# Kernel optimization log

Hardware: AMD Instinct MI355X
Metric: run time of the kernel (lower is better)

The kernel has to match this reference:

```python
import jax, jax.numpy as jnp
import numpy as np

# --- constants (match init_kwargs / input_specs) ---
N_NODES = 32768   # total nodes
N_EDGES = 262144  # total edges (avg degree 8)
B = 512           # number of graphs
D = 64            # node feature / hidden dim (scalar irreps width)
DE = 16           # edge attribute dim
NEXP = 8          # num_experts
K = 2             # top-k


def setup_inputs() -> dict:
    key = jax.random.key(0)
    ks = jax.random.split(key, 20)
    x = jax.random.normal(ks[0], (N_NODES, D), dtype=jnp.float32)
    edge_src = jax.random.randint(ks[1], (N_EDGES,), 0, N_NODES, dtype=jnp.int32)
    edge_dst = jax.random.randint(ks[2], (N_EDGES,), 0, N_NODES, dtype=jnp.int32)
    edge_attr = jax.random.normal(ks[3], (N_EDGES, DE), dtype=jnp.float32)
    # sorted graph ids, every graph non-empty (64 nodes each)
    batch = jnp.repeat(jnp.arange(B, dtype=jnp.int32), N_NODES // B)
    s = 1.0 / np.sqrt(D)
    se = 1.0 / np.sqrt(DE)
    # embedding GNN params
    emb_We = jax.random.normal(ks[4], (DE, D), dtype=jnp.float32) * se
    emb_W1 = jax.random.normal(ks[5], (D, D), dtype=jnp.float32) * s
    emb_W2 = jax.random.normal(ks[6], (D, D), dtype=jnp.float32) * s
    emb_b = jnp.zeros((D,), dtype=jnp.float32)
    # gating network
    Wg = jax.random.normal(ks[7], (D, NEXP), dtype=jnp.float32) * s
    bg = jnp.zeros((NEXP,), dtype=jnp.float32)
    # stacked expert params [NEXP, ...]
    ex_We = jax.random.normal(ks[8], (NEXP, DE, D), dtype=jnp.float32) * se
    ex_W1 = jax.random.normal(ks[9], (NEXP, D, D), dtype=jnp.float32) * s
    ex_W2 = jax.random.normal(ks[10], (NEXP, D, D), dtype=jnp.float32) * s
    ex_b = jnp.zeros((NEXP, D), dtype=jnp.float32)
    ex_Wout = jax.random.normal(ks[11], (NEXP, D, 1), dtype=jnp.float32) * s
    ex_bout = jnp.zeros((NEXP, 1), dtype=jnp.float32)
    return {
        "x": x, "edge_attr": edge_attr,
        "emb_We": emb_We, "emb_W1": emb_W1, "emb_W2": emb_W2, "emb_b": emb_b,
        "Wg": Wg, "bg": bg,
        "ex_We": ex_We, "ex_W1": ex_W1, "ex_W2": ex_W2, "ex_b": ex_b,
        "ex_Wout": ex_Wout, "ex_bout": ex_bout,
        "edge_src": edge_src, "edge_dst": edge_dst, "batch": batch,
    }


def _gnn_embed(x, edge_attr, We, W1, W2, b, src, dst, batch):
    # edge-gated messages: gather x[src], modulate by projected edge attrs, scatter to dst
    msg = x[src] * (edge_attr @ We)                          # [E, D]
    agg = jax.ops.segment_sum(msg, dst, num_segments=N_NODES)  # [N, D]
    h = jax.nn.relu(x @ W1 + agg @ W2 + b)                   # [N, D]
    # mean pooling per graph
    gsum = jax.ops.segment_sum(h, batch, num_segments=B)      # [B, D]
    cnt = jax.ops.segment_sum(jnp.ones((N_NODES, 1), h.dtype), batch, num_segments=B)
    return gsum / jnp.maximum(cnt, 1.0)                      # [B, D]


def _expert(x, edge_attr, We, W1, W2, b, Wout, bout, src, dst, batch):
    emb = _gnn_embed(x, edge_attr, We, W1, W2, b, src, dst, batch)
    return emb @ Wout + bout                                  # [B, 1]


def reference(x, edge_attr, emb_We, emb_W1, emb_W2, emb_b, Wg, bg,
              ex_We, ex_W1, ex_W2, ex_b, ex_Wout, ex_bout,
              edge_src, edge_dst, batch):
    # 1) graph embeddings via embedding GNN
    graph_emb = _gnn_embed(x, edge_attr, emb_We, emb_W1, emb_W2, emb_b,
                           edge_src, edge_dst, batch)          # [B, D]
    # 2) gating: softmax over experts, top-k, renormalize
    routing_weights = jax.nn.softmax(graph_emb @ Wg + bg, axis=1)  # [B, NEXP]
    top_k_weights, top_k_indices = jax.lax.top_k(routing_weights, K)
    norm_top_k = jax.nn.softmax(top_k_weights, axis=1)             # [B, K]
    # 3) dispatch: run every expert on the full batch (vectorized equivalent of
    #    the per-expert masked sub-batch loop), then gather routed outputs
    expert_outs = jax.vmap(
        lambda We, W1, W2, b, Wo, bo: _expert(
            x, edge_attr, We, W1, W2, b, Wo, bo, edge_src, edge_dst, batch)
    )(ex_We, ex_W1, ex_W2, ex_b, ex_Wout, ex_bout)             # [NEXP, B, 1]
    per_graph = expert_outs[:, :, 0].T                         # [B, NEXP]
    gathered = jnp.take_along_axis(per_graph, top_k_indices, axis=1)  # [B, K]
    # 4) weighted combine
    final_output = jnp.sum(gathered * norm_top_k, axis=1, keepdims=True)  # [B, 1]
    return final_output, routing_weights
```

## Files before the change

### kernel.cpp

```cpp
#include <hip/hip_runtime.h>

#define N_NODES 32768
#define N_EDGES 262144
#define NB      512
#define D       64
#define DE      16
#define NEXP    8

typedef __attribute__((ext_vector_type(8))) short  short8v;
typedef __attribute__((ext_vector_type(4))) float  floatx4;

static __device__ __forceinline__ unsigned short f2bf(float f) {
  unsigned int u = __float_as_uint(f);
  u += 0x7FFFu + ((u >> 16) & 1u);
  return (unsigned short)(u >> 16);
}


__global__ void hist_kernel(const int* __restrict__ dst, int* __restrict__ counts) {
  int i = blockIdx.x * blockDim.x + threadIdx.x;
  if (i < N_EDGES) atomicAdd(&counts[dst[i]], 1);
}

__global__ void scan1_kernel(const int* __restrict__ counts, int* __restrict__ offsets,
                             int* __restrict__ bsums) {
  __shared__ int sm[256];
  int t = threadIdx.x, i = blockIdx.x * 256 + t;
  int v = counts[i];
  sm[t] = v;
  __syncthreads();
  for (int off = 1; off < 256; off <<= 1) {
    int u = (t >= off) ? sm[t - off] : 0;
    __syncthreads();
    sm[t] += u;
    __syncthreads();
  }
  offsets[i] = sm[t] - v;
  if (t == 255) bsums[blockIdx.x] = sm[255];
}

__global__ void scan2_kernel(int* __restrict__ bsums) {
  __shared__ int sm[128];
  int t = threadIdx.x;
  int v = bsums[t];
  sm[t] = v;
  __syncthreads();
  for (int off = 1; off < 128; off <<= 1) {
    int u = (t >= off) ? sm[t - off] : 0;
    __syncthreads();
    sm[t] += u;
    __syncthreads();
  }
  bsums[t] = sm[t] - v;
}

__global__ void scan3_kernel(int* __restrict__ offsets, const int* __restrict__ bsums,
                             int* __restrict__ cursor) {
  int i = blockIdx.x * 256 + threadIdx.x;
  int v = offsets[i] + bsums[blockIdx.x];
  offsets[i] = v;
  cursor[i]  = v;
  if (i == 0) offsets[N_NODES] = N_EDGES;
}

__global__ void scatter_kernel(const int* __restrict__ dst, const int* __restrict__ src,
                               const float4* __restrict__ ea4, int* __restrict__ cursor,
                               int* __restrict__ sorted_src, float4* __restrict__ sea4,
                               const float* __restrict__ ex_W1, const float* __restrict__ ex_W2,
                               unsigned short* __restrict__ wpk) {
  int i = blockIdx.x * blockDim.x + threadIdx.x;
  if (i < N_EDGES) {
    int p = atomicAdd(&cursor[dst[i]], 1);
    sorted_src[p] = src[i];
    float4 a = ea4[(size_t)i * 4 + 0];
    float4 b = ea4[(size_t)i * 4 + 1];
    float4 c = ea4[(size_t)i * 4 + 2];
    float4 d = ea4[(size_t)i * 4 + 3];
    sea4[(size_t)p * 4 + 0] = a;
    sea4[(size_t)p * 4 + 1] = b;
    sea4[(size_t)p * 4 + 2] = c;
    sea4[(size_t)p * 4 + 3] = d;
  }
  if (i < NEXP * 2 * D * D) {
    int je  = i >> 13;
    int rem = i & 8191;
    int mat = rem >> 12;
    int cd  = rem & 4095;
    int col = cd >> 6, k = cd & 63;
    const float* W = mat ? ex_W2 : ex_W1;
    wpk[i] = f2bf(W[je * 4096 + k * 64 + col]);
  }
}


__global__ __launch_bounds__(256) void tkern(
    const float* __restrict__ x, const int* __restrict__ sorted_src,
    const float4* __restrict__ sea4, const int* __restrict__ offsets,
    const float* __restrict__ emb_We, float* __restrict__ agg0,
    unsigned int* __restrict__ Tp) {
  int lane = threadIdx.x & 63;
  int wv = threadIdx.x >> 6;
  int n0 = blockIdx.x * 8 + wv * 2;
  int n1 = n0 + 1;
  int st0 = __builtin_amdgcn_readfirstlane(offsets[n0]);
  int en0 = __builtin_amdgcn_readfirstlane(offsets[n0 + 1]);
  int en1 = __builtin_amdgcn_readfirstlane(offsets[n1 + 1]);
  int b0 = st0, b1 = en0;

  float tk0[DE], tk1[DE];
#pragma unroll
  for (int k = 0; k < DE; ++k) { tk0[k] = 0.f; tk1[k] = 0.f; }

  while (b0 < en0 || b1 < en1) {
    int e00 = (b0     < N_EDGES - 1) ? b0     : N_EDGES - 1;
    int e01 = (b0 + 1 < N_EDGES - 1) ? b0 + 1 : N_EDGES - 1;
    int e10 = (b1     < N_EDGES - 1) ? b1     : N_EDGES - 1;
    int e11 = (b1 + 1 < N_EDGES - 1) ? b1 + 1 : N_EDGES - 1;
    float m00 = (b0     < en0) ? 1.f : 0.f;
    float m01 = (b0 + 1 < en0) ? 1.f : 0.f;
    float m10 = (b1     < en1) ? 1.f : 0.f;
    float m11 = (b1 + 1 < en1) ? 1.f : 0.f;
    int s00 = sorted_src[e00];
    int s01 = sorted_src[e01];
    int s10 = sorted_src[e10];
    int s11 = sorted_src[e11];
    const float4* p00 = sea4 + ((size_t)e00 << 2);
    const float4* p01 = sea4 + ((size_t)e01 << 2);
    const float4* p10 = sea4 + ((size_t)e10 << 2);
    const float4* p11 = sea4 + ((size_t)e11 << 2);
    float4 a0 = p00[0], a1 = p00[1], a2 = p00[2], a3 = p00[3];
    float4 c0 = p01[0], c1 = p01[1], c2 = p01[2], c3 = p01[3];
    float4 d0 = p10[0], d1 = p10[1], d2 = p10[2], d3 = p10[3];
    float4 f0 = p11[0], f1 = p11[1], f2 = p11[2], f3 = p11[3];
    float x00 = x[(size_t)s00 * D + lane] * m00;
    float x01 = x[(size_t)s01 * D + lane] * m01;
    float x10 = x[(size_t)s10 * D + lane] * m10;
    float x11 = x[(size_t)s11 * D + lane] * m11;

    tk0[0]  += x00 * a0.x; tk0[1]  += x00 * a0.y; tk0[2]  += x00 * a0.z; tk0[3]  += x00 * a0.w;
    tk0[4]  += x00 * a1.x; tk0[5]  += x00 * a1.y; tk0[6]  += x00 * a1.z; tk0[7]  += x00 * a1.w;
    tk0[8]  += x00 * a2.x; tk0[9]  += x00 * a2.y; tk0[10] += x00 * a2.z; tk0[11] += x00 * a2.w;
    tk0[12] += x00 * a3.x; tk0[13] += x00 * a3.y; tk0[14] += x00 * a3.z; tk0[15] += x00 * a3.w;
    tk0[0]  += x01 * c0.x; tk0[1]  += x01 * c0.y; tk0[2]  += x01 * c0.z; tk0[3]  += x01 * c0.w;
    tk0[4]  += x01 * c1.x; tk0[5]  += x01 * c1.y; tk0[6]  += x01 * c1.z; tk0[7]  += x01 * c1.w;
    tk0[8]  += x01 * c2.x; tk0[9]  += x01 * c2.y; tk0[10] += x01 * c2.z; tk0[11] += x01 * c2.w;
    tk0[12] += x01 * c3.x; tk0[13] += x01 * c3.y; tk0[14] += x01 * c3.z; tk0[15] += x01 * c3.w;
    tk1[0]  += x10 * d0.x; tk1[1]  += x10 * d0.y; tk1[2]  += x10 * d0.z; tk1[3]  += x10 * d0.w;
    tk1[4]  += x10 * d1.x; tk1[5]  += x10 * d1.y; tk1[6]  += x10 * d1.z; tk1[7]  += x10 * d1.w;
    tk1[8]  += x10 * d2.x; tk1[9]  += x10 * d2.y; tk1[10] += x10 * d2.z; tk1[11] += x10 * d2.w;
    tk1[12] += x10 * d3.x; tk1[13] += x10 * d3.y; tk1[14] += x10 * d3.z; tk1[15] += x10 * d3.w;
    tk1[0]  += x11 * f0.x; tk1[1]  += x11 * f0.y; tk1[2]  += x11 * f0.z; tk1[3]  += x11 * f0.w;
    tk1[4]  += x11 * f1.x; tk1[5]  += x11 * f1.y; tk1[6]  += x11 * f1.z; tk1[7]  += x11 * f1.w;
    tk1[8]  += x11 * f2.x; tk1[9]  += x11 * f2.y; tk1[10] += x11 * f2.z; tk1[11] += x11 * f2.w;
    tk1[12] += x11 * f3.x; tk1[13] += x11 * f3.y; tk1[14] += x11 * f3.z; tk1[15] += x11 * f3.w;
    b0 += 2; b1 += 2;
  }

  {
    float av0 = 0.f, av1 = 0.f;
#pragma unroll
    for (int k = 0; k < DE; ++k) {
      float ewk = emb_We[k * D + lane];
      av0 += tk0[k] * ewk;
      av1 += tk1[k] * ewk;
    }
    agg0[(size_t)n0 * D + lane] = av0;
    agg0[(size_t)n1 * D + lane] = av1;
  }
  unsigned int* tp0 = Tp + (size_t)n0 * (D * DE / 2) + lane;
  unsigned int* tp1 = Tp + (size_t)n1 * (D * DE / 2) + lane;
#pragma unroll
  for (int j = 0; j < 8; ++j) {
    unsigned int pk0 = (unsigned int)f2bf(tk0[2 * j]) |
                       ((unsigned int)f2bf(tk0[2 * j + 1]) << 16);
    unsigned int pk1 = (unsigned int)f2bf(tk1[2 * j]) |
                       ((unsigned int)f2bf(tk1[2 * j + 1]) << 16);
    tp0[(size_t)j * D] = pk0;
    tp1[(size_t)j * D] = pk1;
  }
}


__global__ __launch_bounds__(512) void contract_kernel(
    const unsigned int* __restrict__ Tp, const float* __restrict__ ex_We,
    unsigned short* __restrict__ aggb) {
  int lane = threadIdx.x & 63;
  int je = threadIdx.x >> 6;
  float wr[DE];
#pragma unroll
  for (int k = 0; k < DE; ++k) wr[k] = ex_We[(size_t)je * DE * D + k * D + lane];

  int n0 = blockIdx.x * 64;
  unsigned short* ob = aggb + (size_t)je * N_NODES * D;
  for (int i = 0; i < 64; i += 2) {
    int nA = n0 + i, nB = n0 + i + 1;
    const unsigned int* ta = Tp + (size_t)nA * 512 + lane;
    const unsigned int* tb = Tp + (size_t)nB * 512 + lane;
    unsigned int pa0 = ta[0],   pa1 = ta[64],  pa2 = ta[128], pa3 = ta[192];
    unsigned int pa4 = ta[256], pa5 = ta[320], pa6 = ta[384], pa7 = ta[448];
    unsigned int pb0 = tb[0],   pb1 = tb[64],  pb2 = tb[128], pb3 = tb[192];
    unsigned int pb4 = tb[256], pb5 = tb[320], pb6 = tb[384], pb7 = tb[448];
    float sA, sB;
    sA  = __uint_as_float(pa0 << 16)         * wr[0];
    sA += __uint_as_float(pa0 & 0xFFFF0000u) * wr[1];
    sA += __uint_as_float(pa1 << 16)         * wr[2];
    sA += __uint_as_float(pa1 & 0xFFFF0000u) * wr[3];
    sA += __uint_as_float(pa2 << 16)         * wr[4];
    sA += __uint_as_float(pa2 & 0xFFFF0000u) * wr[5];
    sA += __uint_as_float(pa3 << 16)         * wr[6];
    sA += __uint_as_float(pa3 & 0xFFFF0000u) * wr[7];
    sA += __uint_as_float(pa4 << 16)         * wr[8];
    sA += __uint_as_float(pa4 & 0xFFFF0000u) * wr[9];
    sA += __uint_as_float(pa5 << 16)         * wr[10];
    sA += __uint_as_float(pa5 & 0xFFFF0000u) * wr[11];
    sA += __uint_as_float(pa6 << 16)         * wr[12];
    sA += __uint_as_float(pa6 & 0xFFFF0000u) * wr[13];
    sA += __uint_as_float(pa7 << 16)         * wr[14];
    sA += __uint_as_float(pa7 & 0xFFFF0000u) * wr[15];
    sB  = __uint_as_float(pb0 << 16)         * wr[0];
    sB += __uint_as_float(pb0 & 0xFFFF0000u) * wr[1];
    sB += __uint_as_float(pb1 << 16)         * wr[2];
    sB += __uint_as_float(pb1 & 0xFFFF0000u) * wr[3];
    sB += __uint_as_float(pb2 << 16)         * wr[4];
    sB += __uint_as_float(pb2 & 0xFFFF0000u) * wr[5];
    sB += __uint_as_float(pb3 << 16)         * wr[6];
    sB += __uint_as_float(pb3 & 0xFFFF0000u) * wr[7];
    sB += __uint_as_float(pb4 << 16)         * wr[8];
    sB += __uint_as_float(pb4 & 0xFFFF0000u) * wr[9];
    sB += __uint_as_float(pb5 << 16)         * wr[10];
    sB += __uint_as_float(pb5 & 0xFFFF0000u) * wr[11];
    sB += __uint_as_float(pb6 << 16)         * wr[12];
    sB += __uint_as_float(pb6 & 0xFFFF0000u) * wr[13];
    sB += __uint_as_float(pb7 << 16)         * wr[14];
    sB += __uint_as_float(pb7 & 0xFFFF0000u) * wr[15];
    ob[(size_t)nA * D + lane] = f2bf(sA);
    ob[(size_t)nB * D + lane] = f2bf(sB);
  }
}


__global__ __launch_bounds__(256) void gnn0_kernel(
    const float* __restrict__ x, const float* __restrict__ agg0,
    const float* __restrict__ W1, const float* __restrict__ W2,
    const float* __restrict__ bvv, float* __restrict__ graph_emb) {
  __shared__ __align__(16) float w1s[D * D];
  __shared__ __align__(16) float w2s[D * D];
  __shared__ __align__(16) float xs[D * D];
  __shared__ __align__(16) float as2[D * D];
  int b = blockIdx.x;
  int t = threadIdx.x;
  const float4* w1src = (const float4*)W1;
  const float4* w2src = (const float4*)W2;
  const float4* xsrc  = (const float4*)(x    + (size_t)b * D * D);
  const float4* asrc  = (const float4*)(agg0 + (size_t)b * D * D);
#pragma unroll
  for (int r = 0; r < 4; ++r) {
    ((float4*)w1s)[t + r * 256] = w1src[t + r * 256];
    ((float4*)w2s)[t + r * 256] = w2src[t + r * 256];
    ((float4*)xs)[t + r * 256]  = xsrc[t + r * 256];
    ((float4*)as2)[t + r * 256] = asrc[t + r * 256];
  }
  int w = t >> 6, lane = t & 63;
  float bias = bvv[lane];
  __syncthreads();
  float pool = 0.f;
#pragma unroll
  for (int q = 0; q < 4; ++q) {
    int n0 = w * 16 + q * 4;
    float a0 = bias, a1 = bias, a2 = bias, a3 = bias;
#pragma unroll 4
    for (int c4 = 0; c4 < 16; ++c4) {
      float4 x0 = *(const float4*)&xs[(n0 + 0) * D + c4 * 4];
      float4 x1 = *(const float4*)&xs[(n0 + 1) * D + c4 * 4];
      float4 x2 = *(const float4*)&xs[(n0 + 2) * D + c4 * 4];
      float4 x3 = *(const float4*)&xs[(n0 + 3) * D + c4 * 4];
      float4 g0 = *(const float4*)&as2[(n0 + 0) * D + c4 * 4];
      float4 g1 = *(const float4*)&as2[(n0 + 1) * D + c4 * 4];
      float4 g2 = *(const float4*)&as2[(n0 + 2) * D + c4 * 4];
      float4 g3 = *(const float4*)&as2[(n0 + 3) * D + c4 * 4];
      float w10 = w1s[(c4 * 4 + 0) * D + lane];
      float w11 = w1s[(c4 * 4 + 1) * D + lane];
      float w12 = w1s[(c4 * 4 + 2) * D + lane];
      float w13 = w1s[(c4 * 4 + 3) * D + lane];
      float w20 = w2s[(c4 * 4 + 0) * D + lane];
      float w21 = w2s[(c4 * 4 + 1) * D + lane];
      float w22 = w2s[(c4 * 4 + 2) * D + lane];
      float w23 = w2s[(c4 * 4 + 3) * D + lane];
      a0 += x0.x * w10 + x0.y * w11 + x0.z * w12 + x0.w * w13
          + g0.x * w20 + g0.y * w21 + g0.z * w22 + g0.w * w23;
      a1 += x1.x * w10 + x1.y * w11 + x1.z * w12 + x1.w * w13
          + g1.x * w20 + g1.y * w21 + g1.z * w22 + g1.w * w23;
      a2 += x2.x * w10 + x2.y * w11 + x2.z * w12 + x2.w * w13
          + g2.x * w20 + g2.y * w21 + g2.z * w22 + g2.w * w23;
      a3 += x3.x * w10 + x3.y * w11 + x3.z * w12 + x3.w * w13
          + g3.x * w20 + g3.y * w21 + g3.z * w22 + g3.w * w23;
    }
    pool += fmaxf(a0, 0.f) + fmaxf(a1, 0.f) + fmaxf(a2, 0.f) + fmaxf(a3, 0.f);
  }
  __syncthreads();
  xs[w * D + lane] = pool;
  __syncthreads();
  if (w == 0) {
    float s = xs[lane] + xs[D + lane] + xs[2 * D + lane] + xs[3 * D + lane];
    graph_emb[b * D + lane] = s * (1.f / 64.f);
  }
}


__global__ __launch_bounds__(512) void gnn_mfma_kernel(
    const float* __restrict__ x, const unsigned short* __restrict__ aggb,
    const unsigned short* __restrict__ wpk,
    const float* __restrict__ ex_b, const float* __restrict__ ex_Wout,
    const float* __restrict__ ex_bout,
    const float* __restrict__ graph_emb, const float* __restrict__ Wg,
    const float* __restrict__ bg, float* __restrict__ out) {
  __shared__ __align__(16) short xls[4096];
  __shared__ float pg[NEXP];
  __shared__ float lg[NEXP];
  int g = blockIdx.x;
  int t = threadIdx.x;
  {
    const float4* xp = (const float4*)(x + (size_t)g * 4096 + (size_t)t * 8);
    float4 va = xp[0], vb = xp[1];
    short8v pk;
    pk[0] = (short)f2bf(va.x); pk[1] = (short)f2bf(va.y);
    pk[2] = (short)f2bf(va.z); pk[3] = (short)f2bf(va.w);
    pk[4] = (short)f2bf(vb.x); pk[5] = (short)f2bf(vb.y);
    pk[6] = (short)f2bf(vb.z); pk[7] = (short)f2bf(vb.w);
    int row = t >> 3, slot = t & 7;
    *(short8v*)((char*)xls + (((row << 3) + (slot ^ (row & 7))) << 4)) = pk;
  }
  __syncthreads();

  int je = t >> 6;
  int lane = t & 63;
  int r = lane & 15, q = lane >> 4;

  const short* Ab = (const short*)(aggb + ((size_t)je * N_NODES + (size_t)g * D) * D);
  const short* B1 = (const short*)(wpk + (size_t)je * 2 * 4096);
  const short* B2 = B1 + 4096;

  floatx4 acc[4][4];
#pragma unroll
  for (int i = 0; i < 4; ++i)
#pragma unroll
    for (int j = 0; j < 4; ++j) acc[i][j] = (floatx4){0.f, 0.f, 0.f, 0.f};

#pragma unroll
  for (int kk = 0; kk < 2; ++kk) {
    int ko = kk * 32 + q * 8;
    short8v af[4], bf[4];
#pragma unroll
    for (int rt = 0; rt < 4; ++rt) {
      int row = rt * 16 + r;
      int slot = kk * 4 + q;
      af[rt] = *(const short8v*)((char*)xls + (((row << 3) + (slot ^ (row & 7))) << 4));
    }
#pragma unroll
    for (int ct = 0; ct < 4; ++ct) bf[ct] = *(const short8v*)(B1 + (ct * 16 + r) * D + ko);
#pragma unroll
    for (int rt = 0; rt < 4; ++rt)
#pragma unroll
      for (int ct = 0; ct < 4; ++ct)
        acc[rt][ct] = __builtin_amdgcn_mfma_f32_16x16x32_bf16(af[rt], bf[ct], acc[rt][ct], 0, 0, 0);
  }
#pragma unroll
  for (int kk = 0; kk < 2; ++kk) {
    int ko = kk * 32 + q * 8;
    short8v af[4], bf[4];
#pragma unroll
    for (int rt = 0; rt < 4; ++rt) af[rt] = *(const short8v*)(Ab + (rt * 16 + r) * D + ko);
#pragma unroll
    for (int ct = 0; ct < 4; ++ct) bf[ct] = *(const short8v*)(B2 + (ct * 16 + r) * D + ko);
#pragma unroll
    for (int rt = 0; rt < 4; ++rt)
#pragma unroll
      for (int ct = 0; ct < 4; ++ct)
        acc[rt][ct] = __builtin_amdgcn_mfma_f32_16x16x32_bf16(af[rt], bf[ct], acc[rt][ct], 0, 0, 0);
  }

  float o = 0.f;
#pragma unroll
  for (int ct = 0; ct < 4; ++ct) {
    float bcol = ex_b[je * D + ct * 16 + r];
    float s = 0.f;
#pragma unroll
    for (int rt = 0; rt < 4; ++rt)
#pragma unroll
      for (int rg = 0; rg < 4; ++rg) s += fmaxf(acc[rt][ct][rg] + bcol, 0.f);
    s += __shfl_xor(s, 16);
    s += __shfl_xor(s, 32);
    o += s * ex_Wout[je * D + ct * 16 + r];
  }
#pragma unroll
  for (int off = 8; off >= 1; off >>= 1) o += __shfl_xor(o, off);
  if (lane == 0) pg[je] = o * (1.f / 64.f) + ex_bout[je];
  __syncthreads();

  float* es = (float*)xls;
  if (t < 64) es[t] = graph_emb[g * D + t];
  __syncthreads();
  if (t < NEXP) {
    float v = bg[t];
    for (int d = 0; d < D; ++d) v += es[d] * Wg[d * NEXP + t];
    lg[t] = v;
  }
  __syncthreads();
  if (t < NEXP) {
    float l[NEXP];
    float mx = -1e30f;
#pragma unroll
    for (int e = 0; e < NEXP; ++e) { l[e] = lg[e]; mx = fmaxf(mx, l[e]); }
    float p[NEXP];
    float sum = 0.f;
#pragma unroll
    for (int e = 0; e < NEXP; ++e) { p[e] = expf(l[e] - mx); sum += p[e]; }
    float inv = 1.f / sum;
#pragma unroll
    for (int e = 0; e < NEXP; ++e) p[e] *= inv;
    out[NB + g * NEXP + t] = p[t];
    if (t == 0) {
      int i1 = -1; float v1 = -1e30f;
#pragma unroll
      for (int e = 0; e < NEXP; ++e) if (p[e] > v1) { v1 = p[e]; i1 = e; }
      int i2 = -1; float v2 = -1e30f;
#pragma unroll
      for (int e = 0; e < NEXP; ++e) if (e != i1 && p[e] > v2) { v2 = p[e]; i2 = e; }
      float rr = expf(v2 - v1);
      float n1 = 1.f / (1.f + rr);
      float n2 = rr / (1.f + rr);
      out[g] = n1 * pg[i1] + n2 * pg[i2];
    }
  }
}


extern "C" void kernel_launch(void* const* d_in, const int* in_sizes, int n_in,
                              void* d_out, int out_size, void* d_ws, size_t ws_size,
                              hipStream_t stream) {
  const float* x         = (const float*)d_in[0];
  const float* edge_attr = (const float*)d_in[1];
  const float* emb_We    = (const float*)d_in[2];
  const float* emb_W1    = (const float*)d_in[3];
  const float* emb_W2    = (const float*)d_in[4];
  const float* emb_b     = (const float*)d_in[5];
  const float* Wg        = (const float*)d_in[6];
  const float* bg        = (const float*)d_in[7];
  const float* ex_We     = (const float*)d_in[8];
  const float* ex_W1     = (const float*)d_in[9];
  const float* ex_W2     = (const float*)d_in[10];
  const float* ex_b      = (const float*)d_in[11];
  const float* ex_Wout   = (const float*)d_in[12];
  const float* ex_bout   = (const float*)d_in[13];
  const int* edge_src    = (const int*)d_in[14];
  const int* edge_dst    = (const int*)d_in[15];

  char* p = (char*)d_ws;
  auto alloc = [&](size_t bytes) {
    char* q = p;
    p += (bytes + 255) & ~(size_t)255;
    return q;
  };
  int*   counts     = (int*)alloc((size_t)N_NODES * 4);
  int*   offsets    = (int*)alloc((size_t)(N_NODES + 1) * 4);
  int*   cursor     = (int*)alloc((size_t)N_NODES * 4);
  int*   bsums      = (int*)alloc(128 * 4);
  int*   sorted_src = (int*)alloc((size_t)N_EDGES * 4);
  float* sorted_ea  = (float*)alloc((size_t)N_EDGES * DE * 4);
  unsigned int* Tp  = (unsigned int*)alloc((size_t)N_NODES * (D * DE / 2) * 4);
  float* agg0       = (float*)alloc((size_t)N_NODES * D * 4);
  unsigned short* aggb = (unsigned short*)alloc((size_t)NEXP * N_NODES * D * 2);
  unsigned short* wpk  = (unsigned short*)alloc((size_t)NEXP * 2 * D * D * 2);
  float* graph_emb  = (float*)alloc((size_t)NB * D * 4);

  hipMemsetAsync(counts, 0, (size_t)N_NODES * 4, stream);
  hist_kernel<<<N_EDGES / 256, 256, 0, stream>>>(edge_dst, counts);
  scan1_kernel<<<N_NODES / 256, 256, 0, stream>>>(counts, offsets, bsums);
  scan2_kernel<<<1, 128, 0, stream>>>(bsums);
  scan3_kernel<<<N_NODES / 256, 256, 0, stream>>>(offsets, bsums, cursor);
  scatter_kernel<<<N_EDGES / 256, 256, 0, stream>>>(edge_dst, edge_src,
                                                    (const float4*)edge_attr, cursor,
                                                    sorted_src, (float4*)sorted_ea,
                                                    ex_W1, ex_W2, wpk);
  tkern<<<N_NODES / 8, 256, 0, stream>>>(x, sorted_src, (const float4*)sorted_ea,
                                         offsets, emb_We, agg0, Tp);
  contract_kernel<<<N_NODES / 64, 512, 0, stream>>>(Tp, ex_We, aggb);
  gnn0_kernel<<<NB, 256, 0, stream>>>(x, agg0, emb_W1, emb_W2, emb_b, graph_emb);
  gnn_mfma_kernel<<<NB, 512, 0, stream>>>(x, aggb, wpk, ex_b, ex_Wout, ex_bout,
                                          graph_emb, Wg, bg, (float*)d_out);
}
```

Measured before the change: 222.2 us.

## Fuse expert edge-attribute contraction into expert MFMA kernel via LDS staging

Removes the separate contraction kernel that wrote per-expert bf16 aggregated messages for all experts to global memory. Each expert wavefront in the fused kernel now contracts the per-node Tp tensor with its edge weights and writes the result into a swizzled LDS tile, which the second MFMA pass reads. This drops a global write and read of an 8×N×D bf16 buffer and one launch. In exchange the block needs 72 KB of LDS, which may limit occupancy, and the contraction work now sits serially inside the 512-block kernel.

```diff
diff --git a/kernel.cpp b/kernel.cpp
--- a/kernel.cpp
+++ b/kernel.cpp
@@ -177,64 +177,6 @@
                        ((unsigned int)f2bf(tk1[2 * j + 1]) << 16);
     tp0[(size_t)j * D] = pk0;
     tp1[(size_t)j * D] = pk1;
-  }
-}
-
-
-__global__ __launch_bounds__(512) void contract_kernel(
-    const unsigned int* __restrict__ Tp, const float* __restrict__ ex_We,
-    unsigned short* __restrict__ aggb) {
-  int lane = threadIdx.x & 63;
-  int je = threadIdx.x >> 6;
-  float wr[DE];
-#pragma unroll
-  for (int k = 0; k < DE; ++k) wr[k] = ex_We[(size_t)je * DE * D + k * D + lane];
-
-  int n0 = blockIdx.x * 64;
-  unsigned short* ob = aggb + (size_t)je * N_NODES * D;
-  for (int i = 0; i < 64; i += 2) {
-    int nA = n0 + i, nB = n0 + i + 1;
-    const unsigned int* ta = Tp + (size_t)nA * 512 + lane;
-    const unsigned int* tb = Tp + (size_t)nB * 512 + lane;
-    unsigned int pa0 = ta[0],   pa1 = ta[64],  pa2 = ta[128], pa3 = ta[192];
-    unsigned int pa4 = ta[256], pa5 = ta[320], pa6 = ta[384], pa7 = ta[448];
-    unsigned int pb0 = tb[0],   pb1 = tb[64],  pb2 = tb[128], pb3 = tb[192];
-    unsigned int pb4 = tb[256], pb5 = tb[320], pb6 = tb[384], pb7 = tb[448];
-    float sA, sB;
-    sA  = __uint_as_float(pa0 << 16)         * wr[0];
-    sA += __uint_as_float(pa0 & 0xFFFF0000u) * wr[1];
-    sA += __uint_as_float(pa1 << 16)         * wr[2];
-    sA += __uint_as_float(pa1 & 0xFFFF0000u) * wr[3];
-    sA += __uint_as_float(pa2 << 16)         * wr[4];
-    sA += __uint_as_float(pa2 & 0xFFFF0000u) * wr[5];
-    sA += __uint_as_float(pa3 << 16)         * wr[6];
-    sA += __uint_as_float(pa3 & 0xFFFF0000u) * wr[7];
-    sA += __uint_as_float(pa4 << 16)         * wr[8];
-    sA += __uint_as_float(pa4 & 0xFFFF0000u) * wr[9];
-    sA += __uint_as_float(pa5 << 16)         * wr[10];
-    sA += __uint_as_float(pa5 & 0xFFFF0000u) * wr[11];
-    sA += __uint_as_float(pa6 << 16)         * wr[12];
-    sA += __uint_as_float(pa6 & 0xFFFF0000u) * wr[13];
-    sA += __uint_as_float(pa7 << 16)         * wr[14];
-    sA += __uint_as_float(pa7 & 0xFFFF0000u) * wr[15];
-    sB  = __uint_as_float(pb0 << 16)         * wr[0];
-    sB += __uint_as_float(pb0 & 0xFFFF0000u) * wr[1];
-    sB += __uint_as_float(pb1 << 16)         * wr[2];
-    sB += __uint_as_float(pb1 & 0xFFFF0000u) * wr[3];
-    sB += __uint_as_float(pb2 << 16)         * wr[4];
-    sB += __uint_as_float(pb2 & 0xFFFF0000u) * wr[5];
-    sB += __uint_as_float(pb3 << 16)         * wr[6];
-    sB += __uint_as_float(pb3 & 0xFFFF0000u) * wr[7];
-    sB += __uint_as_float(pb4 << 16)         * wr[8];
-    sB += __uint_as_float(pb4 & 0xFFFF0000u) * wr[9];
-    sB += __uint_as_float(pb5 << 16)         * wr[10];
-    sB += __uint_as_float(pb5 & 0xFFFF0000u) * wr[11];
-    sB += __uint_as_float(pb6 << 16)         * wr[12];
-    sB += __uint_as_float(pb6 & 0xFFFF0000u) * wr[13];
-    sB += __uint_as_float(pb7 << 16)         * wr[14];
-    sB += __uint_as_float(pb7 & 0xFFFF0000u) * wr[15];
-    ob[(size_t)nA * D + lane] = f2bf(sA);
-    ob[(size_t)nB * D + lane] = f2bf(sB);
   }
 }
 
@@ -307,14 +249,15 @@
 }
 
 
-__global__ __launch_bounds__(512) void gnn_mfma_kernel(
-    const float* __restrict__ x, const unsigned short* __restrict__ aggb,
-    const unsigned short* __restrict__ wpk,
+__global__ __launch_bounds__(512) void expert_kernel(
+    const float* __restrict__ x, const unsigned int* __restrict__ Tp,
+    const float* __restrict__ ex_We, const unsigned short* __restrict__ wpk,
     const float* __restrict__ ex_b, const float* __restrict__ ex_Wout,
     const float* __restrict__ ex_bout,
     const float* __restrict__ graph_emb, const float* __restrict__ Wg,
     const float* __restrict__ bg, float* __restrict__ out) {
   __shared__ __align__(16) short xls[4096];
+  __shared__ __align__(16) short als[NEXP * 4096];
   __shared__ float pg[NEXP];
   __shared__ float lg[NEXP];
   int g = blockIdx.x;
@@ -330,15 +273,68 @@
     int row = t >> 3, slot = t & 7;
     *(short8v*)((char*)xls + (((row << 3) + (slot ^ (row & 7))) << 4)) = pk;
   }
-  __syncthreads();
 
   int je = t >> 6;
   int lane = t & 63;
+
+  {
+    float wr[DE];
+#pragma unroll
+    for (int k = 0; k < DE; ++k) wr[k] = ex_We[(size_t)je * DE * D + k * D + lane];
+    char* abase = (char*)als + (size_t)je * 8192;
+    int slot = lane >> 3;
+    int within = (lane & 7) << 1;
+    for (int i = 0; i < D; i += 2) {
+      int nA = g * D + i, nB = nA + 1;
+      const unsigned int* ta = Tp + (size_t)nA * 512 + lane;
+      const unsigned int* tb = Tp + (size_t)nB * 512 + lane;
+      unsigned int pa0 = ta[0],   pa1 = ta[64],  pa2 = ta[128], pa3 = ta[192];
+      unsigned int pa4 = ta[256], pa5 = ta[320], pa6 = ta[384], pa7 = ta[448];
+      unsigned int pb0 = tb[0],   pb1 = tb[64],  pb2 = tb[128], pb3 = tb[192];
+      unsigned int pb4 = tb[256], pb5 = tb[320], pb6 = tb[384], pb7 = tb[448];
+      float sA, sB;
+      sA  = __uint_as_float(pa0 << 16)         * wr[0];
+      sA += __uint_as_float(pa0 & 0xFFFF0000u) * wr[1];
+      sA += __uint_as_float(pa1 << 16)         * wr[2];
+      sA += __uint_as_float(pa1 & 0xFFFF0000u) * wr[3];
+      sA += __uint_as_float(pa2 << 16)         * wr[4];
+      sA += __uint_as_float(pa2 & 0xFFFF0000u) * wr[5];
+      sA += __uint_as_float(pa3 << 16)         * wr[6];
+      sA += __uint_as_float(pa3 & 0xFFFF0000u) * wr[7];
+      sA += __uint_as_float(pa4 << 16)         * wr[8];
+      sA += __uint_as_float(pa4 & 0xFFFF0000u) * wr[9];
+      sA += __uint_as_float(pa5 << 16)         * wr[10];
+      sA += __uint_as_float(pa5 & 0xFFFF0000u) * wr[11];
+      sA += __uint_as_float(pa6 << 16)         * wr[12];
+      sA += __uint_as_float(pa6 & 0xFFFF0000u) * wr[13];
+      sA += __uint_as_float(pa7 << 16)         * wr[14];
+      sA += __uint_as_float(pa7 & 0xFFFF0000u) * wr[15];
+      sB  = __uint_as_float(pb0 << 16)         * wr[0];
+      sB += __uint_as_float(pb0 & 0xFFFF0000u) * wr[1];
+      sB += __uint_as_float(pb1 << 16)         * wr[2];
+      sB += __uint_as_float(pb1 & 0xFFFF0000u) * wr[3];
+      sB += __uint_as_float(pb2 << 16)         * wr[4];
+      sB += __uint_as_float(pb2 & 0xFFFF0000u) * wr[5];
+      sB += __uint_as_float(pb3 << 16)         * wr[6];
+      sB += __uint_as_float(pb3 & 0xFFFF0000u) * wr[7];
+      sB += __uint_as_float(pb4 << 16)         * wr[8];
+      sB += __uint_as_float(pb4 & 0xFFFF0000u) * wr[9];
+      sB += __uint_as_float(pb5 << 16)         * wr[10];
+      sB += __uint_as_float(pb5 & 0xFFFF0000u) * wr[11];
+      sB += __uint_as_float(pb6 << 16)         * wr[12];
+      sB += __uint_as_float(pb6 & 0xFFFF0000u) * wr[13];
+      sB += __uint_as_float(pb7 << 16)         * wr[14];
+      sB += __uint_as_float(pb7 & 0xFFFF0000u) * wr[15];
+      *(short*)(abase + (i    ) * 128 + ((slot ^ ( i      & 7)) << 4) + within) = (short)f2bf(sA);
+      *(short*)(abase + (i + 1) * 128 + ((slot ^ ((i + 1) & 7)) << 4) + within) = (short)f2bf(sB);
+    }
+  }
+  __syncthreads();
+
   int r = lane & 15, q = lane >> 4;
-
-  const short* Ab = (const short*)(aggb + ((size_t)je * N_NODES + (size_t)g * D) * D);
   const short* B1 = (const short*)(wpk + (size_t)je * 2 * 4096);
   const short* B2 = B1 + 4096;
+  char* abase = (char*)als + (size_t)je * 8192;
 
   floatx4 acc[4][4];
 #pragma unroll
@@ -369,7 +365,11 @@
     int ko = kk * 32 + q * 8;
     short8v af[4], bf[4];
 #pragma unroll
-    for (int rt = 0; rt < 4; ++rt) af[rt] = *(const short8v*)(Ab + (rt * 16 + r) * D + ko);
+    for (int rt = 0; rt < 4; ++rt) {
+      int row = rt * 16 + r;
+      int slot = kk * 4 + q;
+      af[rt] = *(const short8v*)(abase + (row << 7) + ((slot ^ (row & 7)) << 4));
+    }
 #pragma unroll
     for (int ct = 0; ct < 4; ++ct) bf[ct] = *(const short8v*)(B2 + (ct * 16 + r) * D + ko);
 #pragma unroll
@@ -469,8 +469,7 @@
   float* sorted_ea  = (float*)alloc((size_t)N_EDGES * DE * 4);
   unsigned int* Tp  = (unsigned int*)alloc((size_t)N_NODES * (D * DE / 2) * 4);
   float* agg0       = (float*)alloc((size_t)N_NODES * D * 4);
-  unsigned short* aggb = (unsigned short*)alloc((size_t)NEXP * N_NODES * D * 2);
-  unsigned short* wpk  = (unsigned short*)alloc((size_t)NEXP * 2 * D * D * 2);
+  unsigned short* wpk = (unsigned short*)alloc((size_t)NEXP * 2 * D * D * 2);
   float* graph_emb  = (float*)alloc((size_t)NB * D * 4);
 
   hipMemsetAsync(counts, 0, (size_t)N_NODES * 4, stream);
@@ -484,8 +483,7 @@
                                                     ex_W1, ex_W2, wpk);
   tkern<<<N_NODES / 8, 256, 0, stream>>>(x, sorted_src, (const float4*)sorted_ea,
                                          offsets, emb_We, agg0, Tp);
-  contract_kernel<<<N_NODES / 64, 512, 0, stream>>>(Tp, ex_We, aggb);
   gnn0_kernel<<<NB, 256, 0, stream>>>(x, agg0, emb_W1, emb_W2, emb_b, graph_emb);
-  gnn_mfma_kernel<<<NB, 512, 0, stream>>>(x, aggb, wpk, ex_b, ex_Wout, ex_bout,
-                                          graph_emb, Wg, bg, (float*)d_out);
-}
+  expert_kernel<<<NB, 512, 0, stream>>>(x, Tp, ex_We, wpk, ex_b, ex_Wout, ex_bout,
+                                        graph_emb, Wg, bg, (float*)d_out);
+}
```

Result: faster. 210.2 us (-5.4%).
